# Kernel optimization log

Hardware: AMD Instinct MI355X
Metric: run time of the kernel (lower is better)

The kernel has to match this reference:

```python
import jax, jax.numpy as jnp
import numpy as np

N_NODES = 50000
N_EDGES = 800000
IN_DIM = 128
HID_DIM = 64


def gcn_conv(x, W, b, src, dst, ew):
    """PyG GCNConv with edge_weight: add self-loops (weight 1), symmetric
    normalization D^-1/2 (A+I) D^-1/2, linear transform, scatter-add, bias."""
    n = x.shape[0]
    loop = jnp.arange(n)
    src_a = jnp.concatenate([src, loop])           # [E+N]
    dst_a = jnp.concatenate([dst, loop])
    ew_a = jnp.concatenate([ew, jnp.ones((n,), dtype=x.dtype)])
    deg = jax.ops.segment_sum(ew_a, dst_a, num_segments=n)   # [N]
    dinv = jnp.where(deg > 0, jax.lax.rsqrt(deg), 0.0)
    norm = dinv[src_a] * ew_a * dinv[dst_a]        # [E+N]
    h = x @ W                                      # [N, out]
    msg = h[src_a] * norm[:, None]                 # gather + scale
    out = jax.ops.segment_sum(msg, dst_a, num_segments=n)    # scatter-add
    return out + b


def setup_inputs() -> dict:
    key = jax.random.key(0)
    k = jax.random.split(key, 6)
    x = jax.random.normal(k[0], (N_NODES, IN_DIM), dtype=jnp.float32)
    edge_index = jax.random.randint(k[1], (2, N_EDGES), 0, N_NODES, dtype=jnp.int64)
    edge_weight = jax.random.uniform(k[2], (N_EDGES,), dtype=jnp.float32)
    W1 = jax.random.normal(k[3], (IN_DIM, HID_DIM), dtype=jnp.float32) * (1.0 / np.sqrt(IN_DIM))
    b1 = jnp.zeros((HID_DIM,), dtype=jnp.float32)
    W2 = jax.random.normal(k[4], (HID_DIM, 1), dtype=jnp.float32) * (1.0 / np.sqrt(HID_DIM))
    b2 = jnp.zeros((1,), dtype=jnp.float32)
    return {"x": x, "edge_index": edge_index, "edge_weight": edge_weight,
            "W1": W1, "b1": b1, "W2": W2, "b2": b2}


def reference(x, edge_index, edge_weight, W1, b1, W2, b2):
    src, dst = edge_index[0], edge_index[1]
    h = gcn_conv(x, W1, b1, src, dst, edge_weight)
    h = jax.nn.relu(h)
    h = gcn_conv(h, W2, b2, src, dst, edge_weight)
    return jax.nn.sigmoid(h).squeeze(-1)           # [N]
```

## Files before the change

kernel.cpp:

```cpp
#include <hip/hip_runtime.h>
#include <hip/hip_bf16.h>
#include <math.h>

#define N_NODES 50000
#define N_EDGES 800000
#define IN_DIM  128
#define HID_DIM 64

#define NBKT     196
#define BKT_CAP  5000
#define NPASSC   200
#define EDGES_PER_PASSC (N_EDGES / NPASSC)
#define NGEMM    3125

__global__ __launch_bounds__(256)
void partgemm_kernel(const int* __restrict__ src, const int* __restrict__ dst,
                     const float* __restrict__ ew, int* __restrict__ gcursor,
                     int2* __restrict__ edge_b,
                     const float* __restrict__ x, const float* __restrict__ W1,
                     __hip_bfloat16* __restrict__ h1b) {
    __shared__ float w1s[IN_DIM * HID_DIM];
    __shared__ float xs[16][IN_DIM];
    int bid = blockIdx.x;
    int tid = threadIdx.x;
    if (bid < NPASSC) {
        int* cnt1    = (int*)w1s;
        int* cnt2    = cnt1 + NBKT;
        int* runbase = cnt2 + NBKT;
        if (tid < NBKT) { cnt1[tid] = 0; cnt2[tid] = 0; }
        __syncthreads();
        int e0 = bid * EDGES_PER_PASSC;
        for (int i = tid; i < EDGES_PER_PASSC; i += 256)
            atomicAdd(&cnt1[dst[e0 + i] >> 8], 1);
        __syncthreads();
        if (tid < NBKT) {
            int c = cnt1[tid];
            runbase[tid] = (c > 0) ? atomicAdd(&gcursor[tid], c) : 0;
        }
        __syncthreads();
        for (int i = tid; i < EDGES_PER_PASSC; i += 256) {
            int e = e0 + i;
            int d = dst[e];
            int b = d >> 8;
            int lr = atomicAdd(&cnt2[b], 1);
            int pos = b * BKT_CAP + runbase[b] + lr;
            edge_b[pos] = make_int2(src[e] | ((d & 255) << 16), __float_as_int(ew[e]));
        }
        return;
    }
    int gb = bid - NPASSC;
    const float4* W4 = (const float4*)W1;
    float4* w1s4 = (float4*)w1s;
#pragma unroll
    for (int i = 0; i < 8; ++i) w1s4[tid + 256 * i] = W4[tid + 256 * i];
    int wl = tid >> 6;
    int lane = tid & 63;
    int node0 = gb * 16 + wl * 4;
#pragma unroll
    for (int i = 0; i < 2; ++i) {
        int idx = lane + 64 * i;
        int r = idx >> 5;
        int c = idx & 31;
        ((float4*)xs[wl * 4 + r])[c] = ((const float4*)(x + (long)(node0 + r) * IN_DIM))[c];
    }
    __syncthreads();
    float acc[4] = {0.f, 0.f, 0.f, 0.f};
#pragma unroll 4
    for (int k = 0; k < IN_DIM; k += 4) {
        float4 xv0 = *(const float4*)&xs[wl * 4 + 0][k];
        float4 xv1 = *(const float4*)&xs[wl * 4 + 1][k];
        float4 xv2 = *(const float4*)&xs[wl * 4 + 2][k];
        float4 xv3 = *(const float4*)&xs[wl * 4 + 3][k];
        float w0 = w1s[(k + 0) * HID_DIM + lane];
        float w1 = w1s[(k + 1) * HID_DIM + lane];
        float w2 = w1s[(k + 2) * HID_DIM + lane];
        float w3 = w1s[(k + 3) * HID_DIM + lane];
        acc[0] += xv0.x * w0 + xv0.y * w1 + xv0.z * w2 + xv0.w * w3;
        acc[1] += xv1.x * w0 + xv1.y * w1 + xv1.z * w2 + xv1.w * w3;
        acc[2] += xv2.x * w0 + xv2.y * w1 + xv2.z * w2 + xv2.w * w3;
        acc[3] += xv3.x * w0 + xv3.y * w1 + xv3.z * w2 + xv3.w * w3;
    }
#pragma unroll
    for (int r = 0; r < 4; ++r)
        h1b[(node0 + r) * HID_DIM + lane] = __float2bfloat16(acc[r]);
}

__global__ __launch_bounds__(1024)
void bsort_kernel(const int* __restrict__ gcursor, const int2* __restrict__ edge_b,
                  int2* __restrict__ edge_s, int* __restrict__ start_g,
                  int* __restrict__ cnt_g, float* __restrict__ dinv) {
    __shared__ int   cnt[256];
    __shared__ int   cnt2[256];
    __shared__ float deg[256];
    __shared__ int   sc[256];
    int b   = blockIdx.x;
    int tid = threadIdx.x;
    int M    = gcursor[b];
    int base = b * BKT_CAP;
    if (tid < 256) { cnt[tid] = 0; cnt2[tid] = 0; deg[tid] = 0.0f; }
    __syncthreads();
    for (int i = tid; i < M; i += 1024) {
        int2 e = edge_b[base + i];
        int ld = (e.x >> 16) & 255;
        atomicAdd(&cnt[ld], 1);
        atomicAdd(&deg[ld], __int_as_float(e.y));
    }
    __syncthreads();
    if (tid < 256) sc[tid] = cnt[tid];
    __syncthreads();
#pragma unroll
    for (int off = 1; off < 256; off <<= 1) {
        int t = (tid >= off && tid < 256) ? sc[tid - off] : 0;
        __syncthreads();
        if (tid < 256) sc[tid] += t;
        __syncthreads();
    }
    if (tid < 256) {
        int startL = sc[tid] - cnt[tid];
        int node = b * 256 + tid;
        if (node < N_NODES) {
            start_g[node] = base + startL;
            cnt_g[node]   = cnt[tid];
            dinv[node]    = rsqrtf(1.0f + deg[tid]);
        }
        sc[tid] = startL;
    }
    __syncthreads();
    for (int i = tid; i < M; i += 1024) {
        int2 e = edge_b[base + i];
        int ld = (e.x >> 16) & 255;
        int r = atomicAdd(&cnt2[ld], 1);
        edge_s[base + sc[ld] + r] = make_int2(e.x & 0xFFFF, e.y);
    }
}

__global__ void gather1_layer2_kernel(const int* __restrict__ start_g, const int* __restrict__ cnt_g,
                                      const int2* __restrict__ edge_s,
                                      const __hip_bfloat16* __restrict__ h1b,
                                      const float* __restrict__ dinv, const float* __restrict__ b1,
                                      const float* __restrict__ W2, float* __restrict__ h2s) {
    __shared__ int2 meta[4][64];
    int wave = (blockIdx.x * blockDim.x + threadIdx.x) >> 6;
    int wl = threadIdx.x >> 6;
    int lane = threadIdx.x & 63;
    if (wave >= N_NODES) return;
    int s0 = start_g[wave];
    int ctotal = cnt_g[wave];
    int c0 = (lane & 31) * 2;
    int half = lane >> 5;
    float accA = 0.f, accB = 0.f;
    float accA2 = 0.f, accB2 = 0.f;
    for (int done = 0; done < ctotal; done += 64) {
        int cnt = ctotal - done;
        if (cnt > 64) cnt = 64;
        if (lane < cnt) {
            int2 m = edge_s[s0 + done + lane];
            float w = __int_as_float(m.y) * dinv[m.x];
            meta[wl][lane] = make_int2(m.x, __float_as_int(w));
        }
        __builtin_amdgcn_wave_barrier();
        int cnte = cnt & ~1;
        int j = 0;
        for (; j + 16 <= cnte; j += 16) {
            int2 m0 = meta[wl][j +  0 + half];
            int2 m1 = meta[wl][j +  2 + half];
            int2 m2 = meta[wl][j +  4 + half];
            int2 m3 = meta[wl][j +  6 + half];
            int2 m4 = meta[wl][j +  8 + half];
            int2 m5 = meta[wl][j + 10 + half];
            int2 m6 = meta[wl][j + 12 + half];
            int2 m7 = meta[wl][j + 14 + half];
            unsigned int p0 = *(const unsigned int*)&h1b[m0.x * HID_DIM + c0];
            unsigned int p1 = *(const unsigned int*)&h1b[m1.x * HID_DIM + c0];
            unsigned int p2 = *(const unsigned int*)&h1b[m2.x * HID_DIM + c0];
            unsigned int p3 = *(const unsigned int*)&h1b[m3.x * HID_DIM + c0];
            unsigned int p4 = *(const unsigned int*)&h1b[m4.x * HID_DIM + c0];
            unsigned int p5 = *(const unsigned int*)&h1b[m5.x * HID_DIM + c0];
            unsigned int p6 = *(const unsigned int*)&h1b[m6.x * HID_DIM + c0];
            unsigned int p7 = *(const unsigned int*)&h1b[m7.x * HID_DIM + c0];
            float w0 = __int_as_float(m0.y), w1 = __int_as_float(m1.y);
            float w2 = __int_as_float(m2.y), w3 = __int_as_float(m3.y);
            float w4 = __int_as_float(m4.y), w5 = __int_as_float(m5.y);
            float w6 = __int_as_float(m6.y), w7 = __int_as_float(m7.y);
            accA  += w0 * __uint_as_float(p0 << 16);
            accB  += w0 * __uint_as_float(p0 & 0xFFFF0000u);
            accA2 += w1 * __uint_as_float(p1 << 16);
            accB2 += w1 * __uint_as_float(p1 & 0xFFFF0000u);
            accA  += w2 * __uint_as_float(p2 << 16);
            accB  += w2 * __uint_as_float(p2 & 0xFFFF0000u);
            accA2 += w3 * __uint_as_float(p3 << 16);
            accB2 += w3 * __uint_as_float(p3 & 0xFFFF0000u);
            accA  += w4 * __uint_as_float(p4 << 16);
            accB  += w4 * __uint_as_float(p4 & 0xFFFF0000u);
            accA2 += w5 * __uint_as_float(p5 << 16);
            accB2 += w5 * __uint_as_float(p5 & 0xFFFF0000u);
            accA  += w6 * __uint_as_float(p6 << 16);
            accB  += w6 * __uint_as_float(p6 & 0xFFFF0000u);
            accA2 += w7 * __uint_as_float(p7 << 16);
            accB2 += w7 * __uint_as_float(p7 & 0xFFFF0000u);
        }
        for (; j + 2 <= cnte; j += 2) {
            int2 m = meta[wl][j + half];
            unsigned int p = *(const unsigned int*)&h1b[m.x * HID_DIM + c0];
            accA += __int_as_float(m.y) * __uint_as_float(p << 16);
            accB += __int_as_float(m.y) * __uint_as_float(p & 0xFFFF0000u);
        }
        if (cnt & 1) {
            if (half == 0) {
                int2 m = meta[wl][cnt - 1];
                unsigned int p = *(const unsigned int*)&h1b[m.x * HID_DIM + c0];
                accA += __int_as_float(m.y) * __uint_as_float(p << 16);
                accB += __int_as_float(m.y) * __uint_as_float(p & 0xFFFF0000u);
            }
        }
        __builtin_amdgcn_wave_barrier();
    }
    accA += accA2; accB += accB2;
    accA += __shfl_xor(accA, 32, 64);
    accB += __shfl_xor(accB, 32, 64);
    float di = dinv[wave];
    unsigned int sp = *(const unsigned int*)&h1b[wave * HID_DIM + c0];
    float s0f = __uint_as_float(sp << 16);
    float s1f = __uint_as_float(sp & 0xFFFF0000u);
    float z0 = di * (accA + di * s0f) + b1[c0];
    float z1 = di * (accB + di * s1f) + b1[c0 + 1];
    float h0 = fmaxf(z0, 0.0f);
    float h1v = fmaxf(z1, 0.0f);
    float v = h0 * W2[c0] + h1v * W2[c0 + 1];
#pragma unroll
    for (int off = 16; off > 0; off >>= 1)
        v += __shfl_down(v, off, 32);
    if (lane == 0) h2s[wave] = v * di;
}

__global__ void gather2_final_kernel(const int* __restrict__ start_g, const int* __restrict__ cnt_g,
                                     const int2* __restrict__ edge_s,
                                     const float* __restrict__ h2s, const float* __restrict__ dinv,
                                     const float* __restrict__ b2, float* __restrict__ out) {
    int t = blockIdx.x * blockDim.x + threadIdx.x;
    int n = t >> 4;
    int sub = t & 15;
    if (n >= N_NODES) return;
    int s0 = start_g[n];
    int cnt = cnt_g[n];
    float acc = 0.0f;
    for (int j = sub; j < cnt; j += 16) {
        int2 m = edge_s[s0 + j];
        acc += __int_as_float(m.y) * h2s[m.x];
    }
#pragma unroll
    for (int off = 8; off > 0; off >>= 1)
        acc += __shfl_down(acc, off, 16);
    if (sub == 0) {
        float z = dinv[n] * (acc + h2s[n]) + b2[0];
        out[n] = 1.0f / (1.0f + expf(-z));
    }
}

extern "C" void kernel_launch(void* const* d_in, const int* in_sizes, int n_in,
                              void* d_out, int out_size, void* d_ws, size_t ws_size,
                              hipStream_t stream) {
    const float* x  = (const float*)d_in[0];
    const int*   ei = (const int*)d_in[1];
    const float* ew = (const float*)d_in[2];
    const float* W1 = (const float*)d_in[3];
    const float* b1 = (const float*)d_in[4];
    const float* W2 = (const float*)d_in[5];
    const float* b2 = (const float*)d_in[6];
    float* out = (float*)d_out;

    const int* src = ei;
    const int* dst = ei + N_EDGES;

    char* ws = (char*)d_ws;
    int2*  edge_b  = (int2*)ws;              ws += (size_t)NBKT * BKT_CAP * sizeof(int2);
    int2*  edge_s  = (int2*)ws;              ws += (size_t)NBKT * BKT_CAP * sizeof(int2);
    int*   gcursor = (int*)ws;               ws += NBKT * sizeof(int);
    int*   start_g = (int*)ws;               ws += N_NODES * sizeof(int);
    int*   cnt_g   = (int*)ws;               ws += N_NODES * sizeof(int);
    float* dinv    = (float*)ws;             ws += N_NODES * sizeof(float);
    float* h2s     = (float*)ws;             ws += N_NODES * sizeof(float);
    ws = (char*)(((uintptr_t)ws + 127) & ~(uintptr_t)127);
    __hip_bfloat16* h1b = (__hip_bfloat16*)ws;

    hipMemsetAsync(gcursor, 0, NBKT * sizeof(int), stream);
    partgemm_kernel<<<NPASSC + NGEMM, 256, 0, stream>>>(src, dst, ew, gcursor, edge_b, x, W1, h1b);
    bsort_kernel<<<NBKT, 1024, 0, stream>>>(gcursor, edge_b, edge_s, start_g, cnt_g, dinv);
    gather1_layer2_kernel<<<(N_NODES * 64) / 256, 256, 0, stream>>>(start_g, cnt_g, edge_s, h1b, dinv, b1, W2, h2s);
    gather2_final_kernel<<<(N_NODES * 16 + 255) / 256, 256, 0, stream>>>(start_g, cnt_g, edge_s, h2s, dinv, b2, out);
}
```

Measured before the change: 158.1 us.

## Split GEMM over K across waves with W1 slices held in registers

The X·W1 part of the fused partition/GEMM kernel now has each of the four waves take a 32-wide K slice of W1 into registers. Each wave reads x directly from global memory with wave-uniform addresses and writes partial sums for all 16 nodes to shared memory. A final pass adds the four partials per node and stores bf16 output. This removes the x staging buffer and the repeated per-k LDS reads of W1, at the cost of more registers, an extra barrier and a shared-memory reduction.

```diff
diff --git a/kernel.cpp b/kernel.cpp
--- a/kernel.cpp
+++ b/kernel.cpp
@@ -20,7 +20,6 @@
                      const float* __restrict__ x, const float* __restrict__ W1,
                      __hip_bfloat16* __restrict__ h1b) {
     __shared__ float w1s[IN_DIM * HID_DIM];
-    __shared__ float xs[16][IN_DIM];
     int bid = blockIdx.x;
     int tid = threadIdx.x;
     if (bid < NPASSC) {
@@ -49,40 +48,44 @@
         return;
     }
     int gb = bid - NPASSC;
+    int wv   = tid >> 6;
+    int lane = tid & 63;
+    int node0 = gb * 16;
     const float4* W4 = (const float4*)W1;
     float4* w1s4 = (float4*)w1s;
 #pragma unroll
     for (int i = 0; i < 8; ++i) w1s4[tid + 256 * i] = W4[tid + 256 * i];
-    int wl = tid >> 6;
-    int lane = tid & 63;
-    int node0 = gb * 16 + wl * 4;
-#pragma unroll
-    for (int i = 0; i < 2; ++i) {
-        int idx = lane + 64 * i;
-        int r = idx >> 5;
-        int c = idx & 31;
-        ((float4*)xs[wl * 4 + r])[c] = ((const float4*)(x + (long)(node0 + r) * IN_DIM))[c];
-    }
-    __syncthreads();
-    float acc[4] = {0.f, 0.f, 0.f, 0.f};
-#pragma unroll 4
-    for (int k = 0; k < IN_DIM; k += 4) {
-        float4 xv0 = *(const float4*)&xs[wl * 4 + 0][k];
-        float4 xv1 = *(const float4*)&xs[wl * 4 + 1][k];
-        float4 xv2 = *(const float4*)&xs[wl * 4 + 2][k];
-        float4 xv3 = *(const float4*)&xs[wl * 4 + 3][k];
-        float w0 = w1s[(k + 0) * HID_DIM + lane];
-        float w1 = w1s[(k + 1) * HID_DIM + lane];
-        float w2 = w1s[(k + 2) * HID_DIM + lane];
-        float w3 = w1s[(k + 3) * HID_DIM + lane];
-        acc[0] += xv0.x * w0 + xv0.y * w1 + xv0.z * w2 + xv0.w * w3;
-        acc[1] += xv1.x * w0 + xv1.y * w1 + xv1.z * w2 + xv1.w * w3;
-        acc[2] += xv2.x * w0 + xv2.y * w1 + xv2.z * w2 + xv2.w * w3;
-        acc[3] += xv3.x * w0 + xv3.y * w1 + xv3.z * w2 + xv3.w * w3;
-    }
-#pragma unroll
-    for (int r = 0; r < 4; ++r)
-        h1b[(node0 + r) * HID_DIM + lane] = __float2bfloat16(acc[r]);
+    __syncthreads();
+    int k0 = __builtin_amdgcn_readfirstlane(wv) * 32;
+    float Wreg[32];
+#pragma unroll
+    for (int kk = 0; kk < 32; ++kk) Wreg[kk] = w1s[(k0 + kk) * HID_DIM + lane];
+    __syncthreads();
+    float* psum = w1s;
+    const float* xbase = x + (long)node0 * IN_DIM + k0;
+#pragma unroll
+    for (int n = 0; n < 16; n += 2) {
+        const float4* xa4 = (const float4*)(xbase + (long)n * IN_DIM);
+        const float4* xb4 = (const float4*)(xbase + (long)(n + 1) * IN_DIM);
+        float accA = 0.f, accB = 0.f;
+#pragma unroll
+        for (int q = 0; q < 8; ++q) {
+            float4 xa = xa4[q];
+            float4 xb = xb4[q];
+            accA += xa.x * Wreg[4*q+0] + xa.y * Wreg[4*q+1] + xa.z * Wreg[4*q+2] + xa.w * Wreg[4*q+3];
+            accB += xb.x * Wreg[4*q+0] + xb.y * Wreg[4*q+1] + xb.z * Wreg[4*q+2] + xb.w * Wreg[4*q+3];
+        }
+        psum[(wv * 16 + n) * 64 + lane]     = accA;
+        psum[(wv * 16 + n + 1) * 64 + lane] = accB;
+    }
+    __syncthreads();
+#pragma unroll
+    for (int i = 0; i < 4; ++i) {
+        int n = wv * 4 + i;
+        float s = psum[n * 64 + lane] + psum[(16 + n) * 64 + lane]
+                + psum[(32 + n) * 64 + lane] + psum[(48 + n) * 64 + lane];
+        h1b[(long)(node0 + n) * HID_DIM + lane] = __float2bfloat16(s);
+    }
 }
 
 __global__ __launch_bounds__(1024)
```

Result: slower. 163.2 us (+3.3%).
